# Kernel optimization log

Hardware: AMD Instinct MI355X
Metric: run time of the kernel (lower is better)

The kernel has to match this reference:

```python
import jax, jax.numpy as jnp
import numpy as np

N_NODES = 100000
N_EDGES = 1600000
D_IN = 128
D_HID = 128
N_LAYERS = 3
N_GRAPHS = 128
N_TARGETS = 10
NEG_SLOPE = 0.2


def setup_inputs() -> dict:
    key = jax.random.key(0)
    ks = jax.random.split(key, 12)
    x = jax.random.normal(ks[0], (N_NODES, D_IN), dtype=jnp.float32)
    edge_index = jax.random.randint(ks[1], (2, N_EDGES), 0, N_NODES, dtype=jnp.int64)
    batch = jnp.sort(jax.random.randint(ks[2], (N_NODES,), 0, N_GRAPHS, dtype=jnp.int64))
    # GAT layer params (all layers share shape since D_IN == D_HID)
    s = 1.0 / np.sqrt(D_HID)
    W = jax.random.normal(ks[3], (N_LAYERS, D_IN, D_HID), dtype=jnp.float32) * s
    a_src = jax.random.normal(ks[4], (N_LAYERS, D_HID), dtype=jnp.float32) * s
    a_dst = jax.random.normal(ks[5], (N_LAYERS, D_HID), dtype=jnp.float32) * s
    bias = jnp.zeros((N_LAYERS, D_HID), dtype=jnp.float32)
    # readout MLP: Linear(128,64) + ReLU + Linear(64,10)
    W1 = jax.random.normal(ks[6], (D_HID, 64), dtype=jnp.float32) * s
    b1 = jnp.zeros((64,), dtype=jnp.float32)
    W2 = jax.random.normal(ks[7], (64, N_TARGETS), dtype=jnp.float32) / np.sqrt(64)
    b2 = jnp.zeros((N_TARGETS,), dtype=jnp.float32)
    return {"x": x, "edge_index": edge_index, "batch": batch,
            "W": W, "a_src": a_src, "a_dst": a_dst, "bias": bias,
            "W1": W1, "b1": b1, "W2": W2, "b2": b2}


def _gat_layer(x, src, dst, W_l, a_src_l, a_dst_l, bias_l):
    n = x.shape[0]
    h = x @ W_l                              # [N, D]
    al_s = h @ a_src_l                       # [N]
    al_d = h @ a_dst_l                       # [N]
    e = jax.nn.leaky_relu(al_s[src] + al_d[dst], NEG_SLOPE)  # [E]
    # segment softmax over incoming edges per destination node
    m = jax.ops.segment_max(e, dst, num_segments=n)
    ex = jnp.exp(e - m[dst])
    den = jax.ops.segment_sum(ex, dst, num_segments=n)
    alpha = ex / den[dst]
    out = jax.ops.segment_sum(alpha[:, None] * h[src], dst, num_segments=n)
    return out + bias_l


def reference(x, edge_index, batch, W, a_src, a_dst, bias, W1, b1, W2, b2):
    n = x.shape[0]
    # PyG GATConv default: add self-loops
    loops = jnp.arange(n, dtype=edge_index.dtype)
    src = jnp.concatenate([edge_index[0], loops])
    dst = jnp.concatenate([edge_index[1], loops])
    for l in range(N_LAYERS):
        x = _gat_layer(x, src, dst, W[l], a_src[l], a_dst[l], bias[l])
        # dropout inactive at inference
    g = jax.ops.segment_sum(x, batch, num_segments=N_GRAPHS)  # global_add_pool
    return jax.nn.relu(g @ W1 + b1) @ W2 + b2
```

## Files before the change

kernel.cpp:

```cpp
#include <hip/hip_runtime.h>
#include <math.h>

#define N_NODES 100000
#define N_EDGES 1600000
#define D 128
#define N_LAYERS 3
#define N_GRAPHS 128
#define N_TARGETS 10
#define NEG_SLOPE 0.2f
#define E_TOT (N_EDGES + N_NODES)
#define CSR_W 64

typedef unsigned int u32;
typedef unsigned short u16;
typedef __attribute__((ext_vector_type(8))) short bf16x8;
typedef __attribute__((ext_vector_type(4))) float f32x4;

__device__ __forceinline__ float bf2f(u16 b) {
    u32 u = ((u32)b) << 16;
    return __uint_as_float(u);
}
__device__ __forceinline__ u16 f2bf(float f) {
    u32 u = __float_as_uint(f);
    u32 r = (u + 0x7fffu + ((u >> 16) & 1u)) >> 16;
    return (u16)r;
}

__global__ void build_kernel(const int* __restrict__ src, const int* __restrict__ dst,
                             int* __restrict__ deg, int* __restrict__ csrf) {
    int i = blockIdx.x * blockDim.x + threadIdx.x;
    if (i >= E_TOT) return;
    int s, d;
    if (i < N_EDGES) { s = src[i]; d = dst[i]; } else { s = d = i - N_EDGES; }
    int r = atomicAdd(&deg[d], 1);
    if (r < CSR_W) csrf[d * CSR_W + r] = s;
}

__global__ __launch_bounds__(256) void gemm_kernel(
        const float* __restrict__ X, const float* __restrict__ Wl,
        const float* __restrict__ asr, const float* __restrict__ ads,
        u16* __restrict__ Hb, float* __restrict__ als, float* __restrict__ ald) {
    __shared__ u16 xa[128][136];
    __shared__ u16 wt[128][136];
    int tid = threadIdx.x;
    int row0 = blockIdx.x * 128;

    #pragma unroll
    for (int i = 0; i < 16; ++i) {
        int e = (i * 256 + tid) * 4;
        int r = e >> 7, c = e & 127;
        int row = row0 + r;
        float4 v = make_float4(0.f, 0.f, 0.f, 0.f);
        if (row < N_NODES) v = *(const float4*)&X[(size_t)row * D + c];
        u32 lo = (u32)f2bf(v.x) | ((u32)f2bf(v.y) << 16);
        u32 hi = (u32)f2bf(v.z) | ((u32)f2bf(v.w) << 16);
        *(uint2*)&xa[r][c] = make_uint2(lo, hi);
    }
    #pragma unroll
    for (int i = 0; i < 16; ++i) {
        int e = (i * 256 + tid) * 4;
        int k = e >> 7, c = e & 127;
        float4 v = *(const float4*)&Wl[e];
        wt[c + 0][k] = f2bf(v.x);
        wt[c + 1][k] = f2bf(v.y);
        wt[c + 2][k] = f2bf(v.z);
        wt[c + 3][k] = f2bf(v.w);
    }
    __syncthreads();

    int wv   = tid >> 6;
    int lane = tid & 63;
    int r16  = lane & 15;
    int g    = lane >> 4;
    int rbase = wv * 32;

    f32x4 acc[2][8];
    #pragma unroll
    for (int rt = 0; rt < 2; ++rt)
        #pragma unroll
        for (int ct = 0; ct < 8; ++ct) acc[rt][ct] = (f32x4){0.f, 0.f, 0.f, 0.f};

    #pragma unroll
    for (int kk = 0; kk < 4; ++kk) {
        int k0 = kk * 32 + g * 8;
        bf16x8 bx0 = *(const bf16x8*)&xa[rbase + r16][k0];
        bf16x8 bx1 = *(const bf16x8*)&xa[rbase + 16 + r16][k0];
        #pragma unroll
        for (int ct = 0; ct < 8; ++ct) {
            bf16x8 aw = *(const bf16x8*)&wt[ct * 16 + r16][k0];
            acc[0][ct] = __builtin_amdgcn_mfma_f32_16x16x32_bf16(aw, bx0, acc[0][ct], 0, 0, 0);
            acc[1][ct] = __builtin_amdgcn_mfma_f32_16x16x32_bf16(aw, bx1, acc[1][ct], 0, 0, 0);
        }
    }

    #pragma unroll
    for (int rt = 0; rt < 2; ++rt) {
        int row = row0 + rbase + rt * 16 + r16;
        float ps = 0.f, pd = 0.f;
        #pragma unroll
        for (int ct = 0; ct < 8; ++ct) {
            float4 av = *(const float4*)&asr[ct * 16 + g * 4];
            float4 dv = *(const float4*)&ads[ct * 16 + g * 4];
            f32x4 a = acc[rt][ct];
            ps += a[0] * av.x + a[1] * av.y + a[2] * av.z + a[3] * av.w;
            pd += a[0] * dv.x + a[1] * dv.y + a[2] * dv.z + a[3] * dv.w;
        }
        ps += __shfl_xor(ps, 16); ps += __shfl_xor(ps, 32);
        pd += __shfl_xor(pd, 16); pd += __shfl_xor(pd, 32);
        if (row < N_NODES) {
            #pragma unroll
            for (int ct = 0; ct < 8; ++ct) {
                f32x4 a = acc[rt][ct];
                u32 lo = (u32)f2bf(a[0]) | ((u32)f2bf(a[1]) << 16);
                u32 hi = (u32)f2bf(a[2]) | ((u32)f2bf(a[3]) << 16);
                *(uint2*)&Hb[(size_t)row * D + ct * 16 + g * 4] = make_uint2(lo, hi);
            }
            if (g == 0) { als[row] = ps; ald[row] = pd; }
        }
    }
}

__global__ __launch_bounds__(256) void edge_kernel(
        const u16* __restrict__ hb, const float* __restrict__ als,
        const float* __restrict__ ald, const int* __restrict__ deg_arr,
        const int* __restrict__ csrf, const float* __restrict__ bias,
        const int* __restrict__ esrc, const int* __restrict__ edst,
        float* __restrict__ out) {
    int gtid = blockIdx.x * blockDim.x + threadIdx.x;
    int node = gtid >> 6;
    int lane = threadIdx.x & 63;
    if (node >= N_NODES) return;
    int deg = deg_arr[node];
    float ad = ald[node];
    float accx = 0.f, accy = 0.f;
    const u16* hl = hb + lane * 2;

    if (deg <= CSR_W) {
        int sreg = 0;
        float v = -3.0e38f;
        if (lane < deg) {
            sreg = csrf[node * CSR_W + lane];
            float t = als[sreg] + ad;
            v = (t > 0.f) ? t : NEG_SLOPE * t;
        }
        float m = v;
        #pragma unroll
        for (int o = 1; o < 64; o <<= 1) m = fmaxf(m, __shfl_xor(m, o));
        float w = (lane < deg) ? __expf(v - m) : 0.f;
        float sum = w;
        #pragma unroll
        for (int o = 1; o < 64; o <<= 1) sum += __shfl_xor(sum, o);
        w *= 1.f / sum;

        int e = 0;
        for (; e + 8 <= deg; e += 8) {
            int s[8]; float wv[8]; ushort2 hv[8];
            #pragma unroll
            for (int k = 0; k < 8; ++k) { s[k] = __shfl(sreg, e + k); wv[k] = __shfl(w, e + k); }
            #pragma unroll
            for (int k = 0; k < 8; ++k) hv[k] = *(const ushort2*)(hl + (size_t)s[k] * D);
            #pragma unroll
            for (int k = 0; k < 8; ++k) {
                accx += wv[k] * bf2f(hv[k].x);
                accy += wv[k] * bf2f(hv[k].y);
            }
        }
        for (; e < deg; ++e) {
            int s0 = __shfl(sreg, e);
            float w0 = __shfl(w, e);
            ushort2 h0 = *(const ushort2*)(hl + (size_t)s0 * D);
            accx += w0 * bf2f(h0.x);
            accy += w0 * bf2f(h0.y);
        }
    } else {
        float lm = -3.0e38f;
        for (int j = lane; j < E_TOT; j += 64) {
            int d = (j < N_EDGES) ? edst[j] : (j - N_EDGES);
            if (d == node) {
                int s = (j < N_EDGES) ? esrc[j] : (j - N_EDGES);
                float t = als[s] + ad;
                t = (t > 0.f) ? t : NEG_SLOPE * t;
                lm = fmaxf(lm, t);
            }
        }
        #pragma unroll
        for (int o = 1; o < 64; o <<= 1) lm = fmaxf(lm, __shfl_xor(lm, o));
        float m = lm;
        float lsum = 0.f;
        for (int j = lane; j < E_TOT; j += 64) {
            int d = (j < N_EDGES) ? edst[j] : (j - N_EDGES);
            if (d == node) {
                int s = (j < N_EDGES) ? esrc[j] : (j - N_EDGES);
                float t = als[s] + ad;
                t = (t > 0.f) ? t : NEG_SLOPE * t;
                lsum += __expf(t - m);
            }
        }
        #pragma unroll
        for (int o = 1; o < 64; o <<= 1) lsum += __shfl_xor(lsum, o);
        float invden = 1.f / lsum;
        for (int base = 0; base < E_TOT; base += 64) {
            int j = base + lane;
            int d = -1;
            if (j < E_TOT) d = (j < N_EDGES) ? edst[j] : (j - N_EDGES);
            unsigned long long mask = __ballot(d == node);
            while (mask) {
                int b = __ffsll(mask) - 1;
                mask &= mask - 1;
                int jj = base + b;
                int s = (jj < N_EDGES) ? esrc[jj] : (jj - N_EDGES);
                float t = als[s] + ad;
                t = (t > 0.f) ? t : NEG_SLOPE * t;
                float w = __expf(t - m) * invden;
                ushort2 hv = *(const ushort2*)(hl + (size_t)s * D);
                accx += w * bf2f(hv.x);
                accy += w * bf2f(hv.y);
            }
        }
    }

    float2 bv = *(const float2*)(bias + lane * 2);
    *(float2*)(out + (size_t)node * D + lane * 2) = make_float2(accx + bv.x, accy + bv.y);
}

__global__ void bounds_kernel(const int* __restrict__ batch, int* __restrict__ gstart) {
    int g = blockIdx.x * blockDim.x + threadIdx.x;
    if (g > N_GRAPHS) return;
    if (g == N_GRAPHS) { gstart[g] = N_NODES; return; }
    int lo = 0, hi = N_NODES;
    while (lo < hi) { int mid = (lo + hi) >> 1; if (batch[mid] < g) lo = mid + 1; else hi = mid; }
    gstart[g] = lo;
}

__global__ void pool_kernel(const float* __restrict__ x, const int* __restrict__ gstart,
                            float* __restrict__ gpool) {
    int g = blockIdx.x >> 3, c = blockIdx.x & 7;
    int t = threadIdx.x;
    int beg = gstart[g], end = gstart[g + 1];
    float acc = 0.f;
    for (int i = beg + c; i < end; i += 8) acc += x[(size_t)i * D + t];
    atomicAdd(&gpool[g * D + t], acc);
}

__global__ void readout_kernel(const float* __restrict__ gpool,
                               const float* __restrict__ W1, const float* __restrict__ b1,
                               const float* __restrict__ W2, const float* __restrict__ b2,
                               float* __restrict__ out) {
    int g = blockIdx.x;
    int t = threadIdx.x;
    __shared__ float hid[64];
    float a = b1[t];
    for (int k = 0; k < D; ++k) a += gpool[g * D + k] * W1[k * 64 + t];
    hid[t] = fmaxf(a, 0.f);
    __syncthreads();
    if (t < N_TARGETS) {
        float o = b2[t];
        for (int k = 0; k < 64; ++k) o += hid[k] * W2[k * N_TARGETS + t];
        out[g * N_TARGETS + t] = o;
    }
}

extern "C" void kernel_launch(void* const* d_in, const int* in_sizes, int n_in,
                              void* d_out, int out_size, void* d_ws, size_t ws_size,
                              hipStream_t stream) {
    const float* x    = (const float*)d_in[0];
    const int*   ei   = (const int*)d_in[1];
    const int*   batch= (const int*)d_in[2];
    const float* W    = (const float*)d_in[3];
    const float* a_s  = (const float*)d_in[4];
    const float* a_d  = (const float*)d_in[5];
    const float* bias = (const float*)d_in[6];
    const float* W1   = (const float*)d_in[7];
    const float* b1   = (const float*)d_in[8];
    const float* W2   = (const float*)d_in[9];
    const float* b2   = (const float*)d_in[10];
    float* out = (float*)d_out;
    const int* srcp = ei;
    const int* dstp = ei + N_EDGES;

    char* p = (char*)d_ws;
    float* bufA = (float*)p; p += (size_t)N_NODES * D * 4;
    float* bufB = (float*)p; p += (size_t)N_NODES * D * 4;
    u16* hb     = (u16*)p;   p += (size_t)N_NODES * D * 2;
    int* csrf   = (int*)p;   p += (size_t)N_NODES * CSR_W * 4;
    float* als  = (float*)p; p += (size_t)N_NODES * 4;
    float* ald  = (float*)p; p += (size_t)N_NODES * 4;
    int* deg    = (int*)p;   p += (size_t)N_NODES * 4;
    int* gstart = (int*)p;   p += 132 * 4;
    float* gpool = (float*)p; p += N_GRAPHS * D * 4;

    hipMemsetAsync(deg, 0, N_NODES * 4, stream);
    hipMemsetAsync(gpool, 0, N_GRAPHS * D * 4, stream);

    int eb = (E_TOT + 255) / 256;
    build_kernel<<<eb, 256, 0, stream>>>(srcp, dstp, deg, csrf);
    bounds_kernel<<<1, 256, 0, stream>>>(batch, gstart);

    const float* cur = x;
    float* outs[3] = {bufA, bufB, bufA};
    for (int l = 0; l < N_LAYERS; ++l) {
        gemm_kernel<<<(N_NODES + 127) / 128, 256, 0, stream>>>(
            cur, W + (size_t)l * D * D, a_s + (size_t)l * D, a_d + (size_t)l * D,
            hb, als, ald);
        edge_kernel<<<(N_NODES * 64 + 255) / 256, 256, 0, stream>>>(
            hb, als, ald, deg, csrf, bias + (size_t)l * D, srcp, dstp, outs[l]);
        cur = outs[l];
    }
    pool_kernel<<<N_GRAPHS * 8, 128, 0, stream>>>(cur, gstart, gpool);
    readout_kernel<<<N_GRAPHS, 64, 0, stream>>>(gpool, W1, b1, W2, b2, out);
}
```

Baseline: 605.4 us.

## Build compact CSR via two-level bucket sort instead of padded atomic slots

Replaces the padded fixed-width adjacency build (global atomics per edge, 64 slots per node) with a two-pass bucket sort: a block histogram over 256 destination buckets, a scan, a scatter into a temporary buffer, then a per-bucket local counting sort in shared memory that writes a compact CSR with offsets. The edge kernel reads from this CSR, and the high-degree fallback now walks only its own neighbors instead of scanning the full edge list. This removes global atomic contention and the scattered writes into a large padded array, and keeps each node's neighbor list contiguous and sorted in dst order. The cost is four extra kernel launches, reuse of bufB as scratch, and a single-block scan.

```diff
diff --git a/kernel.cpp b/kernel.cpp
--- a/kernel.cpp
+++ b/kernel.cpp
@@ -9,7 +9,11 @@
 #define N_TARGETS 10
 #define NEG_SLOPE 0.2f
 #define E_TOT (N_EDGES + N_NODES)
-#define CSR_W 64
+
+#define NBK 256
+#define BKT_NODES 391
+#define CHUNK 6641
+#define SEG_CAP 8192
 
 typedef unsigned int u32;
 typedef unsigned short u16;
@@ -26,14 +30,125 @@
     return (u16)r;
 }
 
-__global__ void build_kernel(const int* __restrict__ src, const int* __restrict__ dst,
-                             int* __restrict__ deg, int* __restrict__ csrf) {
-    int i = blockIdx.x * blockDim.x + threadIdx.x;
-    if (i >= E_TOT) return;
-    int s, d;
-    if (i < N_EDGES) { s = src[i]; d = dst[i]; } else { s = d = i - N_EDGES; }
-    int r = atomicAdd(&deg[d], 1);
-    if (r < CSR_W) csrf[d * CSR_W + r] = s;
+__global__ __launch_bounds__(256) void histA_kernel(const int* __restrict__ dst,
+                                                    int* __restrict__ cntg) {
+    __shared__ int c[NBK];
+    int blk = blockIdx.x, tid = threadIdx.x;
+    c[tid] = 0;
+    __syncthreads();
+    int base = blk * CHUNK;
+    int end = base + CHUNK; if (end > E_TOT) end = E_TOT;
+    for (int i = base + tid; i < end; i += 256) {
+        int d = (i < N_EDGES) ? dst[i] : (i - N_EDGES);
+        atomicAdd(&c[d / BKT_NODES], 1);
+    }
+    __syncthreads();
+    cntg[blk * NBK + tid] = c[tid];
+}
+
+__global__ __launch_bounds__(256) void scanA_kernel(int* __restrict__ cntg,
+                                                    int* __restrict__ bucket_base) {
+    __shared__ int tot[NBK];
+    __shared__ int sc[NBK];
+    int b = threadIdx.x;
+    int sum = 0;
+    for (int blk = 0; blk < 256; ++blk) {
+        int v = cntg[blk * NBK + b];
+        cntg[blk * NBK + b] = sum;
+        sum += v;
+    }
+    tot[b] = sum;
+    sc[b] = sum;
+    __syncthreads();
+    for (int o = 1; o < NBK; o <<= 1) {
+        int x = (b >= o) ? sc[b - o] : 0;
+        __syncthreads();
+        sc[b] += x;
+        __syncthreads();
+    }
+    int excl = sc[b] - tot[b];
+    bucket_base[b] = excl;
+    if (b == NBK - 1) bucket_base[NBK] = excl + tot[b];
+    for (int blk = 0; blk < 256; ++blk) cntg[blk * NBK + b] += excl;
+}
+
+__global__ __launch_bounds__(256) void scatA_kernel(const int* __restrict__ src,
+                                                    const int* __restrict__ dst,
+                                                    const int* __restrict__ cntg,
+                                                    uint2* __restrict__ tmp) {
+    __shared__ int off[NBK];
+    __shared__ int c2[NBK];
+    int blk = blockIdx.x, tid = threadIdx.x;
+    off[tid] = cntg[blk * NBK + tid];
+    c2[tid] = 0;
+    __syncthreads();
+    int base = blk * CHUNK;
+    int end = base + CHUNK; if (end > E_TOT) end = E_TOT;
+    for (int i = base + tid; i < end; i += 256) {
+        int s, d;
+        if (i < N_EDGES) { s = src[i]; d = dst[i]; } else { s = d = i - N_EDGES; }
+        int b = d / BKT_NODES;
+        int r = atomicAdd(&c2[b], 1);
+        tmp[off[b] + r] = make_uint2((u32)s, (u32)d);
+    }
+}
+
+__global__ __launch_bounds__(256) void bucketB_kernel(const uint2* __restrict__ tmp,
+                                                      const int* __restrict__ bucket_base,
+                                                      int* __restrict__ offg,
+                                                      int* __restrict__ csr) {
+    __shared__ int dcnt[BKT_NODES + 1];
+    __shared__ int lro[BKT_NODES + 1];
+    __shared__ int psum[256];
+    __shared__ int srow[SEG_CAP];
+    int b = blockIdx.x, tid = threadIdx.x;
+    int dbase = b * BKT_NODES;
+    int nb = N_NODES - dbase; if (nb > BKT_NODES) nb = BKT_NODES;
+    int beg = bucket_base[b], end = bucket_base[b + 1];
+    int len = end - beg;
+
+    for (int i = tid; i < BKT_NODES + 1; i += 256) dcnt[i] = 0;
+    __syncthreads();
+    for (int i = tid; i < len; i += 256) {
+        uint2 e = tmp[beg + i];
+        atomicAdd(&dcnt[(int)e.y - dbase], 1);
+    }
+    __syncthreads();
+    int a0 = (2 * tid     < nb) ? dcnt[2 * tid]     : 0;
+    int a1 = (2 * tid + 1 < nb) ? dcnt[2 * tid + 1] : 0;
+    psum[tid] = a0 + a1;
+    __syncthreads();
+    for (int o = 1; o < 256; o <<= 1) {
+        int x = (tid >= o) ? psum[tid - o] : 0;
+        __syncthreads();
+        psum[tid] += x;
+        __syncthreads();
+    }
+    int excl = psum[tid] - (a0 + a1);
+    if (2 * tid     < nb) lro[2 * tid]     = excl;
+    if (2 * tid + 1 < nb) lro[2 * tid + 1] = excl + a0;
+    __syncthreads();
+    for (int i = tid; i < nb; i += 256) offg[dbase + i] = beg + lro[i];
+    if (b == 0 && tid == 0) offg[N_NODES] = E_TOT;
+    for (int i = tid; i < nb; i += 256) dcnt[i] = 0;
+    __syncthreads();
+    if (len <= SEG_CAP) {
+        for (int i = tid; i < len; i += 256) {
+            uint2 e = tmp[beg + i];
+            int dl = (int)e.y - dbase;
+            int r = atomicAdd(&dcnt[dl], 1);
+            srow[lro[dl] + r] = (int)e.x;
+        }
+        __syncthreads();
+        for (int i = tid; i < len; i += 256) csr[beg + i] = srow[i];
+    } else {
+        for (int i = tid; i < len; i += 256) {
+            uint2 e = tmp[beg + i];
+            int dl = (int)e.y - dbase;
+            int r = atomicAdd(&dcnt[dl], 1);
+            csr[beg + lro[dl] + r] = (int)e.x;
+        }
+    }
 }
 
 __global__ __launch_bounds__(256) void gemm_kernel(
@@ -122,24 +237,24 @@
 
 __global__ __launch_bounds__(256) void edge_kernel(
         const u16* __restrict__ hb, const float* __restrict__ als,
-        const float* __restrict__ ald, const int* __restrict__ deg_arr,
-        const int* __restrict__ csrf, const float* __restrict__ bias,
-        const int* __restrict__ esrc, const int* __restrict__ edst,
+        const float* __restrict__ ald, const int* __restrict__ off,
+        const int* __restrict__ csr, const float* __restrict__ bias,
         float* __restrict__ out) {
     int gtid = blockIdx.x * blockDim.x + threadIdx.x;
     int node = gtid >> 6;
     int lane = threadIdx.x & 63;
     if (node >= N_NODES) return;
-    int deg = deg_arr[node];
+    int beg = off[node], end = off[node + 1];
+    int deg = end - beg;
     float ad = ald[node];
     float accx = 0.f, accy = 0.f;
     const u16* hl = hb + lane * 2;
 
-    if (deg <= CSR_W) {
+    if (deg <= 64) {
         int sreg = 0;
         float v = -3.0e38f;
         if (lane < deg) {
-            sreg = csrf[node * CSR_W + lane];
+            sreg = csr[beg + lane];
             float t = als[sreg] + ad;
             v = (t > 0.f) ? t : NEG_SLOPE * t;
         }
@@ -174,48 +289,33 @@
         }
     } else {
         float lm = -3.0e38f;
-        for (int j = lane; j < E_TOT; j += 64) {
-            int d = (j < N_EDGES) ? edst[j] : (j - N_EDGES);
-            if (d == node) {
-                int s = (j < N_EDGES) ? esrc[j] : (j - N_EDGES);
-                float t = als[s] + ad;
-                t = (t > 0.f) ? t : NEG_SLOPE * t;
-                lm = fmaxf(lm, t);
-            }
+        for (int j = lane; j < deg; j += 64) {
+            int s = csr[beg + j];
+            float t = als[s] + ad;
+            t = (t > 0.f) ? t : NEG_SLOPE * t;
+            lm = fmaxf(lm, t);
         }
         #pragma unroll
         for (int o = 1; o < 64; o <<= 1) lm = fmaxf(lm, __shfl_xor(lm, o));
         float m = lm;
         float lsum = 0.f;
-        for (int j = lane; j < E_TOT; j += 64) {
-            int d = (j < N_EDGES) ? edst[j] : (j - N_EDGES);
-            if (d == node) {
-                int s = (j < N_EDGES) ? esrc[j] : (j - N_EDGES);
-                float t = als[s] + ad;
-                t = (t > 0.f) ? t : NEG_SLOPE * t;
-                lsum += __expf(t - m);
-            }
+        for (int j = lane; j < deg; j += 64) {
+            int s = csr[beg + j];
+            float t = als[s] + ad;
+            t = (t > 0.f) ? t : NEG_SLOPE * t;
+            lsum += __expf(t - m);
         }
         #pragma unroll
         for (int o = 1; o < 64; o <<= 1) lsum += __shfl_xor(lsum, o);
         float invden = 1.f / lsum;
-        for (int base = 0; base < E_TOT; base += 64) {
-            int j = base + lane;
-            int d = -1;
-            if (j < E_TOT) d = (j < N_EDGES) ? edst[j] : (j - N_EDGES);
-            unsigned long long mask = __ballot(d == node);
-            while (mask) {
-                int b = __ffsll(mask) - 1;
-                mask &= mask - 1;
-                int jj = base + b;
-                int s = (jj < N_EDGES) ? esrc[jj] : (jj - N_EDGES);
-                float t = als[s] + ad;
-                t = (t > 0.f) ? t : NEG_SLOPE * t;
-                float w = __expf(t - m) * invden;
-                ushort2 hv = *(const ushort2*)(hl + (size_t)s * D);
-                accx += w * bf2f(hv.x);
-                accy += w * bf2f(hv.y);
-            }
+        for (int e = 0; e < deg; ++e) {
+            int s = csr[beg + e];
+            float t = als[s] + ad;
+            t = (t > 0.f) ? t : NEG_SLOPE * t;
+            float w = __expf(t - m) * invden;
+            ushort2 hv = *(const ushort2*)(hl + (size_t)s * D);
+            accx += w * bf2f(hv.x);
+            accy += w * bf2f(hv.y);
         }
     }
 
@@ -282,18 +382,22 @@
     float* bufA = (float*)p; p += (size_t)N_NODES * D * 4;
     float* bufB = (float*)p; p += (size_t)N_NODES * D * 4;
     u16* hb     = (u16*)p;   p += (size_t)N_NODES * D * 2;
-    int* csrf   = (int*)p;   p += (size_t)N_NODES * CSR_W * 4;
+    int* csr    = (int*)p;   p += (size_t)E_TOT * 4;
+    int* offg   = (int*)p;   p += (size_t)(N_NODES + 1) * 4;
     float* als  = (float*)p; p += (size_t)N_NODES * 4;
     float* ald  = (float*)p; p += (size_t)N_NODES * 4;
-    int* deg    = (int*)p;   p += (size_t)N_NODES * 4;
+    int* cntg   = (int*)p;   p += 256 * NBK * 4;
+    int* bucket_base = (int*)p; p += (NBK + 1) * 4;
     int* gstart = (int*)p;   p += 132 * 4;
     float* gpool = (float*)p; p += N_GRAPHS * D * 4;
-
-    hipMemsetAsync(deg, 0, N_NODES * 4, stream);
+    uint2* tmp = (uint2*)bufB;
+
     hipMemsetAsync(gpool, 0, N_GRAPHS * D * 4, stream);
 
-    int eb = (E_TOT + 255) / 256;
-    build_kernel<<<eb, 256, 0, stream>>>(srcp, dstp, deg, csrf);
+    histA_kernel<<<256, 256, 0, stream>>>(dstp, cntg);
+    scanA_kernel<<<1, 256, 0, stream>>>(cntg, bucket_base);
+    scatA_kernel<<<256, 256, 0, stream>>>(srcp, dstp, cntg, tmp);
+    bucketB_kernel<<<NBK, 256, 0, stream>>>(tmp, bucket_base, offg, csr);
     bounds_kernel<<<1, 256, 0, stream>>>(batch, gstart);
 
     const float* cur = x;
@@ -303,7 +407,7 @@
             cur, W + (size_t)l * D * D, a_s + (size_t)l * D, a_d + (size_t)l * D,
             hb, als, ald);
         edge_kernel<<<(N_NODES * 64 + 255) / 256, 256, 0, stream>>>(
-            hb, als, ald, deg, csrf, bias + (size_t)l * D, srcp, dstp, outs[l]);
+            hb, als, ald, offg, csr, bias + (size_t)l * D, outs[l]);
         cur = outs[l];
     }
     pool_kernel<<<N_GRAPHS * 8, 128, 0, stream>>>(cur, gstart, gpool);
```

After: 562.8 us. -7.0%, faster.
